# Optimization experiments

Measured on AMD Instinct MI355X. Metric: run time of the kernel, lower is better.

Reference implementation:

```python
import jax, jax.numpy as jnp
import numpy as np

B, N, K = 16, 2048, 16          # clouds, points per cloud, knn k
C_IN, C_OUT = 64, 64

def setup_inputs() -> dict:
    key = jax.random.key(0)
    ks = jax.random.split(key, 8)
    s_in = 1.0 / np.sqrt(C_IN)
    return {
        "x": jax.random.normal(ks[0], (B * N, C_IN), jnp.float32),
        "pos": jax.random.normal(ks[1], (B * N, 3), jnp.float32),
        "batch": jnp.repeat(jnp.arange(B, dtype=jnp.int32), N),
        "W_pos": jax.random.normal(ks[2], (3, C_OUT), jnp.float32) / np.sqrt(3.0),
        "b_pos": jnp.zeros((C_OUT,), jnp.float32),
        "W_attn": jax.random.normal(ks[3], (C_OUT, C_OUT), jnp.float32) / np.sqrt(C_OUT),
        "b_attn": jnp.zeros((C_OUT,), jnp.float32),
        "W_val": jax.random.normal(ks[4], (C_IN, C_OUT), jnp.float32) * s_in,
        "W_src": jax.random.normal(ks[5], (C_IN, C_OUT), jnp.float32) * s_in,
        "W_dst": jax.random.normal(ks[6], (C_IN, C_OUT), jnp.float32) * s_in,
    }

def _gather(a, idx):
    # a: [B, N, D], idx: [B, N, K+1] -> [B, N, K+1, D]
    return jax.vmap(lambda ab, ib: ab[ib])(a, idx)

def reference(x, pos, batch, W_pos, b_pos, W_attn, b_attn, W_val, W_src, W_dst):
    # batch is assumed contiguous with equal-size clouds (B clouds of N points),
    # so batch-restricted knn_graph == per-cloud knn after reshape.
    posr = pos.reshape(B, N, 3)
    xr = x.reshape(B, N, C_IN)
    # knn_graph(loop=False): exclude self, then PointTransformerConv re-adds self loops
    d2 = jnp.sum((posr[:, :, None, :] - posr[:, None, :, :]) ** 2, axis=-1)  # [B,N,N]
    d2 = d2 + jnp.eye(N, dtype=d2.dtype) * 1e10
    _, nbr = jax.lax.top_k(-d2, K)                                # [B,N,K] sources j per target i
    self_idx = jnp.broadcast_to(jnp.arange(N)[None, :, None], (B, N, 1))
    nbr = jnp.concatenate([nbr, self_idx], axis=2)                # self loop -> [B,N,K+1]
    alpha_i = xr @ W_dst                                          # lin_dst(x_i)  [B,N,C_OUT]
    alpha_j = _gather(xr @ W_src, nbr)                            # lin_src(x_j)  [B,N,K+1,C_OUT]
    val_j = _gather(xr @ W_val, nbr)                              # lin(x_j)
    pos_j = _gather(posr, nbr)                                    # [B,N,K+1,3]
    delta = (posr[:, :, None, :] - pos_j) @ W_pos + b_pos         # pos_nn(pos_i - pos_j)
    alpha = alpha_i[:, :, None, :] - alpha_j + delta              # subtraction attention
    alpha = alpha @ W_attn + b_attn                               # attn_nn
    alpha = jax.nn.softmax(alpha, axis=2)                         # segment softmax per target i
    out = jnp.sum(alpha * (val_j + delta), axis=2)                # weighted scatter-sum
    return out.reshape(B * N, C_OUT)
```

## Files before the change

### kernel.cpp

```cpp
#include <hip/hip_runtime.h>
#include <math.h>

#define BBATCH 16
#define NPC    2048
#define KNBR   16
#define NPTS   (BBATCH*NPC)
#define NGEMM  512
#define NKNN   512
#define BUFCAP 512

__global__ __launch_bounds__(1024) void prep_kernel(
    const float* __restrict__ Wpos, const float* __restrict__ bpos,
    const float* __restrict__ Wattn, const float* __restrict__ battn,
    const float* __restrict__ Wsrc, const float* __restrict__ Wdst,
    float* __restrict__ Hd, float* __restrict__ Hs,
    float* __restrict__ WP2, float* __restrict__ bb) {
  __shared__ float sW[4096];
  __shared__ float sD[4096];
  __shared__ float sS[4096];
  int t = threadIdx.x;
  ((float4*)sW)[t] = ((const float4*)Wattn)[t];
  ((float4*)sD)[t] = ((const float4*)Wdst)[t];
  ((float4*)sS)[t] = ((const float4*)Wsrc)[t];
  __syncthreads();
  int c = t & 63, r0 = t >> 6;
#pragma unroll
  for (int q = 0; q < 4; ++q) {
    int r = r0 + 16 * q;
    float ad = 0.f, as = 0.f;
    for (int d = 0; d < 64; ++d) {
      float w = sW[d * 64 + c];
      ad += sD[r * 64 + d] * w;
      as += sS[r * 64 + d] * w;
    }
    Hd[r * 64 + c] = ad;
    Hs[r * 64 + c] = as;
  }
  if (t < 64) {
    for (int rr = 0; rr < 3; ++rr) {
      float a = 0.f;
      for (int d = 0; d < 64; ++d) a += Wpos[rr * 64 + d] * sW[d * 64 + t];
      WP2[rr * 64 + t] = a;
    }
    float a = battn[t];
    for (int d = 0; d < 64; ++d) a += bpos[d] * sW[d * 64 + t];
    bb[t] = a;
  }
}

__global__ __launch_bounds__(1024) void fused_gk_kernel(
    const float* __restrict__ pos, const float* __restrict__ x,
    const float* __restrict__ Hd, const float* __restrict__ Hs,
    const float* __restrict__ Wval,
    int* __restrict__ nbr, float* __restrict__ A2, float* __restrict__ S2,
    float* __restrict__ V) {
  __shared__ __align__(16) char smem[65536];
  int t = threadIdx.x;
  int bid = blockIdx.x;
  int c = t & 63, g = t >> 6;

  if (bid < NGEMM) {
    float* R0 = (float*)smem;
    float* R1 = (float*)(smem + 16384);
    float* R2 = (float*)(smem + 32768);
    float* R3 = (float*)(smem + 49152);
    ((float4*)R0)[t] = ((const float4*)(x + (size_t)bid * 64 * 64))[t];
    ((float4*)R1)[t] = ((const float4*)Hd)[t];
    ((float4*)R2)[t] = ((const float4*)Hs)[t];
    ((float4*)R3)[t] = ((const float4*)Wval)[t];
    __syncthreads();

    float v0 = 0, v1 = 0, v2 = 0, v3 = 0;
    float a0 = 0, a1 = 0, a2 = 0, a3 = 0;
    float s0 = 0, s1 = 0, s2 = 0, s3 = 0;
    const float4* xr0 = (const float4*)(R0 + (g * 4 + 0) * 64);
    const float4* xr1 = (const float4*)(R0 + (g * 4 + 1) * 64);
    const float4* xr2 = (const float4*)(R0 + (g * 4 + 2) * 64);
    const float4* xr3 = (const float4*)(R0 + (g * 4 + 3) * 64);
#pragma unroll 4
    for (int k4 = 0; k4 < 16; ++k4) {
      float4 q0 = xr0[k4], q1 = xr1[k4], q2 = xr2[k4], q3 = xr3[k4];
#pragma unroll
      for (int kk = 0; kk < 4; ++kk) {
        int k = k4 * 4 + kk;
        float wv = R3[k * 64 + c];
        float wa = R1[k * 64 + c];
        float ws = R2[k * 64 + c];
        float e0 = (kk == 0) ? q0.x : (kk == 1) ? q0.y : (kk == 2) ? q0.z : q0.w;
        float e1 = (kk == 0) ? q1.x : (kk == 1) ? q1.y : (kk == 2) ? q1.z : q1.w;
        float e2 = (kk == 0) ? q2.x : (kk == 1) ? q2.y : (kk == 2) ? q2.z : q2.w;
        float e3 = (kk == 0) ? q3.x : (kk == 1) ? q3.y : (kk == 2) ? q3.z : q3.w;
        v0 += e0 * wv; v1 += e1 * wv; v2 += e2 * wv; v3 += e3 * wv;
        a0 += e0 * wa; a1 += e1 * wa; a2 += e2 * wa; a3 += e3 * wa;
        s0 += e0 * ws; s1 += e1 * ws; s2 += e2 * ws; s3 += e3 * ws;
      }
    }
    size_t o0 = ((size_t)bid * 64 + g * 4 + 0) * 64 + c;
    V[o0] = v0; A2[o0] = a0; S2[o0] = s0;
    size_t o1 = o0 + 64;  V[o1] = v1; A2[o1] = a1; S2[o1] = s1;
    size_t o2 = o0 + 128; V[o2] = v2; A2[o2] = a2; S2[o2] = s2;
    size_t o3 = o0 + 192; V[o3] = v3; A2[o3] = a3; S2[o3] = s3;
    return;
  }

  int kb = bid - NGEMM;
  float4* pos4 = (float4*)smem;
  unsigned short* buf = (unsigned short*)(smem + 32768);
  int cloud = kb >> 5;
  const float* pc = pos + (size_t)cloud * NPC * 3;
  for (int p = t; p < NPC; p += 1024)
    pos4[p] = make_float4(pc[3 * p], pc[3 * p + 1], pc[3 * p + 2], 0.f);
  __syncthreads();

  int w = g, lane = c;
  for (int u = 0; u < 4; ++u) {
    int lt = u * 16 + w;
    int gi = kb * 64 + lt;
    int ti = gi & (NPC - 1);
    float4 tp = pos4[ti];
    float tx = tp.x, ty = tp.y, tz = tp.z;

    int bkt[32];
#pragma unroll
    for (int cc = 0; cc < 32; ++cc) {
      int j = cc * 64 + lane;
      float4 q = pos4[j];
      float dx = tx - q.x, dy = ty - q.y, dz = tz - q.z;
      float d2 = dx * dx + dy * dy + dz * dz;
      int b = (int)(__float_as_uint(d2) >> 20) - 896;
      bkt[cc] = max(0, min(255, b));
    }

    int lo = 0, hi = 255;
    for (int it = 0; it < 8; ++it) {
      int mid = (lo + hi) >> 1;
      int cnt = 0;
#pragma unroll
      for (int cc = 0; cc < 32; ++cc)
        cnt += (int)__popcll(__ballot(bkt[cc] <= mid));
      if (cnt >= 17) hi = mid; else lo = mid + 1;
    }
    int Tp1 = min(hi + 1, 255);

    int base = 0;
#pragma unroll
    for (int cc = 0; cc < 32; ++cc) {
      bool f = (bkt[cc] <= Tp1);
      unsigned long long mm = __ballot(f);
      unsigned int pre = __builtin_amdgcn_mbcnt_hi(
          (unsigned)(mm >> 32), __builtin_amdgcn_mbcnt_lo((unsigned)mm, 0u));
      if (f) {
        int p = base + (int)pre;
        if (p < BUFCAP) buf[w * BUFCAP + p] = (unsigned short)(cc * 64 + lane);
      }
      base += (int)__popcll(mm);
    }
    int n = min(base, BUFCAP);
    double txd = (double)tx, tyd = (double)ty, tzd = (double)tz;

    if (n <= 64) {
      unsigned long long gb = 0xFFFFFFFFFFFFFFFFull;
      int gj = 0x40000000 + lane;
      if (lane < n) {
        int j = buf[w * BUFCAP + lane];
        if (j != ti) {
          float4 q = pos4[j];
          double dx = __dsub_rn(txd, (double)q.x);
          double dy = __dsub_rn(tyd, (double)q.y);
          double dz = __dsub_rn(tzd, (double)q.z);
          double d2 = __dadd_rn(__dadd_rn(__dmul_rn(dx, dx), __dmul_rn(dy, dy)),
                                __dmul_rn(dz, dz));
          gb = (unsigned long long)__double_as_longlong(d2);
          gj = j;
        }
      }
      for (int k = 2; k <= 64; k <<= 1) {
        for (int jj = k >> 1; jj > 0; jj >>= 1) {
          unsigned long long ob = __shfl_xor(gb, jj);
          int oj = __shfl_xor(gj, jj);
          bool keepmin = (((lane & k) == 0) == ((lane & jj) == 0));
          bool less = (ob < gb) || (ob == gb && oj < gj);
          if (keepmin == less) { gb = ob; gj = oj; }
        }
      }
      if (lane < KNBR) nbr[(size_t)gi * KNBR + lane] = gj;
    } else {
      unsigned long long kb2[8];
      int id2[8];
#pragma unroll
      for (int r = 0; r < 8; ++r) {
        int e = r * 64 + lane;
        kb2[r] = 0xFFFFFFFFFFFFFFFFull;
        id2[r] = 0x40000000 + e;
        if (e < n) {
          int j = buf[w * BUFCAP + e];
          if (j != ti) {
            float4 q = pos4[j];
            double dx = __dsub_rn(txd, (double)q.x);
            double dy = __dsub_rn(tyd, (double)q.y);
            double dz = __dsub_rn(tzd, (double)q.z);
            double d2 = __dadd_rn(
                __dadd_rn(__dmul_rn(dx, dx), __dmul_rn(dy, dy)),
                __dmul_rn(dz, dz));
            kb2[r] = (unsigned long long)__double_as_longlong(d2);
            id2[r] = j;
          }
        }
      }
      for (int r = 0; r < KNBR; ++r) {
        unsigned long long lb = kb2[0];
        int lj = id2[0];
#pragma unroll
        for (int cc = 1; cc < 8; ++cc)
          if (kb2[cc] < lb || (kb2[cc] == lb && id2[cc] < lj)) {
            lb = kb2[cc]; lj = id2[cc];
          }
        unsigned long long gb2 = lb;
        int gj2 = lj;
#pragma unroll
        for (int d = 32; d >= 1; d >>= 1) {
          unsigned long long ob = __shfl_xor(gb2, d);
          int oj = __shfl_xor(gj2, d);
          if (ob < gb2 || (ob == gb2 && oj < gj2)) { gb2 = ob; gj2 = oj; }
        }
#pragma unroll
        for (int cc = 0; cc < 8; ++cc)
          if (id2[cc] == gj2) kb2[cc] = 0xFFFFFFFFFFFFFFFFull;
        if (lane == 0) nbr[(size_t)gi * KNBR + r] = gj2;
      }
    }
  }
}

__global__ __launch_bounds__(256) void edge_kernel(
    const float* __restrict__ pos, const int* __restrict__ nbr,
    const float* __restrict__ A2, const float* __restrict__ S2,
    const float* __restrict__ V, const float* __restrict__ WP2,
    const float* __restrict__ bbv, const float* __restrict__ Wpos,
    const float* __restrict__ bpos, float* __restrict__ out) {
  int t = threadIdx.x, w = t >> 6, c = t & 63;
  int bid = blockIdx.x;
  int xcd = bid & 7, slot = bid >> 3;
  int cloud = xcd + 8 * (slot >> 9);
  int cb = slot & 511;
  int gi = cloud * NPC + cb * 4 + w;
  int cloudbase = gi & ~(NPC - 1);
  float pix = pos[(size_t)gi * 3], piy = pos[(size_t)gi * 3 + 1],
        piz = pos[(size_t)gi * 3 + 2];
  float a2 = A2[(size_t)gi * 64 + c];
  float wp0 = WP2[c], wp1 = WP2[64 + c], wp2 = WP2[128 + c], bbc = bbv[c];
  float u0 = Wpos[c], u1 = Wpos[64 + c], u2 = Wpos[128 + c], bpc = bpos[c];

  float lg[17], vl[17];
#pragma unroll
  for (int e = 0; e < 17; ++e) {
    int j = (e < 16) ? nbr[(size_t)gi * KNBR + e] : (gi & (NPC - 1));
    int jg = cloudbase + j;
    float dx = pix - pos[(size_t)jg * 3];
    float dy = piy - pos[(size_t)jg * 3 + 1];
    float dz = piz - pos[(size_t)jg * 3 + 2];
    float s2 = S2[(size_t)jg * 64 + c];
    float v = V[(size_t)jg * 64 + c];
    lg[e] = a2 - s2 + dx * wp0 + dy * wp1 + dz * wp2 + bbc;
    vl[e] = v + dx * u0 + dy * u1 + dz * u2 + bpc;
  }
  float mx = lg[0];
#pragma unroll
  for (int e = 1; e < 17; ++e) mx = fmaxf(mx, lg[e]);
  float den = 0.f, acc = 0.f;
#pragma unroll
  for (int e = 0; e < 17; ++e) {
    float wgt = __expf(lg[e] - mx);
    den += wgt;
    acc += wgt * vl[e];
  }
  out[(size_t)gi * 64 + c] = acc / den;
}

extern "C" void kernel_launch(void* const* d_in, const int* in_sizes, int n_in,
                              void* d_out, int out_size, void* d_ws, size_t ws_size,
                              hipStream_t stream) {
  const float* x     = (const float*)d_in[0];
  const float* pos   = (const float*)d_in[1];
  const float* Wpos  = (const float*)d_in[3];
  const float* bpos  = (const float*)d_in[4];
  const float* Wattn = (const float*)d_in[5];
  const float* battn = (const float*)d_in[6];
  const float* Wval  = (const float*)d_in[7];
  const float* Wsrc  = (const float*)d_in[8];
  const float* Wdst  = (const float*)d_in[9];

  float* ws  = (float*)d_ws;
  float* A2  = ws;
  float* S2  = A2 + (size_t)NPTS * 64;
  float* V   = S2 + (size_t)NPTS * 64;
  float* WP2 = V + (size_t)NPTS * 64;
  float* bb  = WP2 + 192;
  int*   nbr = (int*)(bb + 64);
  float* Hd  = (float*)(nbr + (size_t)NPTS * KNBR);
  float* Hs  = Hd + 4096;
  float* out = (float*)d_out;

  prep_kernel<<<1, 1024, 0, stream>>>(Wpos, bpos, Wattn, battn, Wsrc, Wdst,
                                      Hd, Hs, WP2, bb);
  fused_gk_kernel<<<NGEMM + NKNN, 1024, 0, stream>>>(
      pos, x, Hd, Hs, Wval, nbr, A2, S2, V);
  edge_kernel<<<NPTS / 4, 256, 0, stream>>>(pos, nbr, A2, S2, V, WP2, bb,
                                            Wpos, bpos, out);
}
```

Measured before the change: 223.5 us.

## Interleave S2/V into one buffer, SoA positions in LDS, linear edge block order

Stores the source-projection and value rows interleaved as float2 in a single buffer, so each neighbor gather in the edge kernel is one 8-byte load instead of two separate 4-byte loads from different arrays. The kNN stage now keeps positions in LDS as separate x/y/z arrays rather than padded float4s, which cuts LDS use and changes the bank access pattern. The edge kernel drops its XCD-aware cloud remapping in favor of a plain linear block-to-point mapping. The last change can lower L2 locality per XCD, since blocks from one cloud are no longer pinned to the same die.

```diff
diff --git a/kernel.cpp b/kernel.cpp
--- a/kernel.cpp
+++ b/kernel.cpp
@@ -52,8 +52,7 @@
     const float* __restrict__ pos, const float* __restrict__ x,
     const float* __restrict__ Hd, const float* __restrict__ Hs,
     const float* __restrict__ Wval,
-    int* __restrict__ nbr, float* __restrict__ A2, float* __restrict__ S2,
-    float* __restrict__ V) {
+    int* __restrict__ nbr, float* __restrict__ A2, float* __restrict__ IL) {
   __shared__ __align__(16) char smem[65536];
   int t = threadIdx.x;
   int bid = blockIdx.x;
@@ -95,21 +94,30 @@
         s0 += e0 * ws; s1 += e1 * ws; s2 += e2 * ws; s3 += e3 * ws;
       }
     }
-    size_t o0 = ((size_t)bid * 64 + g * 4 + 0) * 64 + c;
-    V[o0] = v0; A2[o0] = a0; S2[o0] = s0;
-    size_t o1 = o0 + 64;  V[o1] = v1; A2[o1] = a1; S2[o1] = s1;
-    size_t o2 = o0 + 128; V[o2] = v2; A2[o2] = a2; S2[o2] = s2;
-    size_t o3 = o0 + 192; V[o3] = v3; A2[o3] = a3; S2[o3] = s3;
+    size_t row = (size_t)bid * 64 + g * 4;
+    A2[(row + 0) * 64 + c] = a0;
+    A2[(row + 1) * 64 + c] = a1;
+    A2[(row + 2) * 64 + c] = a2;
+    A2[(row + 3) * 64 + c] = a3;
+    ((float2*)(IL + (row + 0) * 128))[c] = make_float2(s0, v0);
+    ((float2*)(IL + (row + 1) * 128))[c] = make_float2(s1, v1);
+    ((float2*)(IL + (row + 2) * 128))[c] = make_float2(s2, v2);
+    ((float2*)(IL + (row + 3) * 128))[c] = make_float2(s3, v3);
     return;
   }
 
   int kb = bid - NGEMM;
-  float4* pos4 = (float4*)smem;
-  unsigned short* buf = (unsigned short*)(smem + 32768);
+  float* px = (float*)smem;
+  float* py = (float*)(smem + 8192);
+  float* pz = (float*)(smem + 16384);
+  unsigned short* buf = (unsigned short*)(smem + 24576);
   int cloud = kb >> 5;
   const float* pc = pos + (size_t)cloud * NPC * 3;
-  for (int p = t; p < NPC; p += 1024)
-    pos4[p] = make_float4(pc[3 * p], pc[3 * p + 1], pc[3 * p + 2], 0.f);
+  for (int p = t; p < NPC; p += 1024) {
+    px[p] = pc[3 * p];
+    py[p] = pc[3 * p + 1];
+    pz[p] = pc[3 * p + 2];
+  }
   __syncthreads();
 
   int w = g, lane = c;
@@ -117,15 +125,13 @@
     int lt = u * 16 + w;
     int gi = kb * 64 + lt;
     int ti = gi & (NPC - 1);
-    float4 tp = pos4[ti];
-    float tx = tp.x, ty = tp.y, tz = tp.z;
+    float tx = px[ti], ty = py[ti], tz = pz[ti];
 
     int bkt[32];
 #pragma unroll
     for (int cc = 0; cc < 32; ++cc) {
       int j = cc * 64 + lane;
-      float4 q = pos4[j];
-      float dx = tx - q.x, dy = ty - q.y, dz = tz - q.z;
+      float dx = tx - px[j], dy = ty - py[j], dz = tz - pz[j];
       float d2 = dx * dx + dy * dy + dz * dz;
       int b = (int)(__float_as_uint(d2) >> 20) - 896;
       bkt[cc] = max(0, min(255, b));
@@ -164,10 +170,9 @@
       if (lane < n) {
         int j = buf[w * BUFCAP + lane];
         if (j != ti) {
-          float4 q = pos4[j];
-          double dx = __dsub_rn(txd, (double)q.x);
-          double dy = __dsub_rn(tyd, (double)q.y);
-          double dz = __dsub_rn(tzd, (double)q.z);
+          double dx = __dsub_rn(txd, (double)px[j]);
+          double dy = __dsub_rn(tyd, (double)py[j]);
+          double dz = __dsub_rn(tzd, (double)pz[j]);
           double d2 = __dadd_rn(__dadd_rn(__dmul_rn(dx, dx), __dmul_rn(dy, dy)),
                                 __dmul_rn(dz, dz));
           gb = (unsigned long long)__double_as_longlong(d2);
@@ -195,10 +200,9 @@
         if (e < n) {
           int j = buf[w * BUFCAP + e];
           if (j != ti) {
-            float4 q = pos4[j];
-            double dx = __dsub_rn(txd, (double)q.x);
-            double dy = __dsub_rn(tyd, (double)q.y);
-            double dz = __dsub_rn(tzd, (double)q.z);
+            double dx = __dsub_rn(txd, (double)px[j]);
+            double dy = __dsub_rn(tyd, (double)py[j]);
+            double dz = __dsub_rn(tzd, (double)pz[j]);
             double d2 = __dadd_rn(
                 __dadd_rn(__dmul_rn(dx, dx), __dmul_rn(dy, dy)),
                 __dmul_rn(dz, dz));
@@ -234,16 +238,12 @@
 
 __global__ __launch_bounds__(256) void edge_kernel(
     const float* __restrict__ pos, const int* __restrict__ nbr,
-    const float* __restrict__ A2, const float* __restrict__ S2,
-    const float* __restrict__ V, const float* __restrict__ WP2,
-    const float* __restrict__ bbv, const float* __restrict__ Wpos,
-    const float* __restrict__ bpos, float* __restrict__ out) {
+    const float* __restrict__ A2, const float* __restrict__ IL,
+    const float* __restrict__ WP2, const float* __restrict__ bbv,
+    const float* __restrict__ Wpos, const float* __restrict__ bpos,
+    float* __restrict__ out) {
   int t = threadIdx.x, w = t >> 6, c = t & 63;
-  int bid = blockIdx.x;
-  int xcd = bid & 7, slot = bid >> 3;
-  int cloud = xcd + 8 * (slot >> 9);
-  int cb = slot & 511;
-  int gi = cloud * NPC + cb * 4 + w;
+  int gi = blockIdx.x * 4 + w;
   int cloudbase = gi & ~(NPC - 1);
   float pix = pos[(size_t)gi * 3], piy = pos[(size_t)gi * 3 + 1],
         piz = pos[(size_t)gi * 3 + 2];
@@ -259,10 +259,9 @@
     float dx = pix - pos[(size_t)jg * 3];
     float dy = piy - pos[(size_t)jg * 3 + 1];
     float dz = piz - pos[(size_t)jg * 3 + 2];
-    float s2 = S2[(size_t)jg * 64 + c];
-    float v = V[(size_t)jg * 64 + c];
-    lg[e] = a2 - s2 + dx * wp0 + dy * wp1 + dz * wp2 + bbc;
-    vl[e] = v + dx * u0 + dy * u1 + dz * u2 + bpc;
+    float2 sv = *(const float2*)(IL + (size_t)jg * 128 + 2 * c);
+    lg[e] = a2 - sv.x + dx * wp0 + dy * wp1 + dz * wp2 + bbc;
+    vl[e] = sv.y + dx * u0 + dy * u1 + dz * u2 + bpc;
   }
   float mx = lg[0];
 #pragma unroll
@@ -292,9 +291,8 @@
 
   float* ws  = (float*)d_ws;
   float* A2  = ws;
-  float* S2  = A2 + (size_t)NPTS * 64;
-  float* V   = S2 + (size_t)NPTS * 64;
-  float* WP2 = V + (size_t)NPTS * 64;
+  float* IL  = A2 + (size_t)NPTS * 64;
+  float* WP2 = IL + (size_t)NPTS * 128;
   float* bb  = WP2 + 192;
   int*   nbr = (int*)(bb + 64);
   float* Hd  = (float*)(nbr + (size_t)NPTS * KNBR);
@@ -304,7 +302,7 @@
   prep_kernel<<<1, 1024, 0, stream>>>(Wpos, bpos, Wattn, battn, Wsrc, Wdst,
                                       Hd, Hs, WP2, bb);
   fused_gk_kernel<<<NGEMM + NKNN, 1024, 0, stream>>>(
-      pos, x, Hd, Hs, Wval, nbr, A2, S2, V);
-  edge_kernel<<<NPTS / 4, 256, 0, stream>>>(pos, nbr, A2, S2, V, WP2, bb,
+      pos, x, Hd, Hs, Wval, nbr, A2, IL);
+  edge_kernel<<<NPTS / 4, 256, 0, stream>>>(pos, nbr, A2, IL, WP2, bb,
                                             Wpos, bpos, out);
 }
```

After: 279.7 us. 1.25x slower.

## Split fused GEMM/KNN kernel into separate kernels with XCD-aware block mapping

Applied to the files above, without the earlier changes.

Splits the combined GEMM+KNN launch into two separate kernels, each launched with its own grid. Both kernels remap block IDs so that blocks of the same cloud land on the same XCD. The KNN kernel also stores positions as SoA arrays in shared memory instead of padded float4. This is meant to cut the shared-memory footprint and register pressure of the fused kernel and improve cache locality, but it adds a launch and serializes two phases that previously could run concurrently.

```diff
diff --git a/kernel.cpp b/kernel.cpp
--- a/kernel.cpp
+++ b/kernel.cpp
@@ -48,68 +48,79 @@
   }
 }
 
-__global__ __launch_bounds__(1024) void fused_gk_kernel(
-    const float* __restrict__ pos, const float* __restrict__ x,
-    const float* __restrict__ Hd, const float* __restrict__ Hs,
-    const float* __restrict__ Wval,
-    int* __restrict__ nbr, float* __restrict__ A2, float* __restrict__ S2,
-    float* __restrict__ V) {
-  __shared__ __align__(16) char smem[65536];
+__global__ __launch_bounds__(1024, 8) void gemm_kernel(
+    const float* __restrict__ x, const float* __restrict__ Hd,
+    const float* __restrict__ Hs, const float* __restrict__ Wval,
+    float* __restrict__ A2, float* __restrict__ S2, float* __restrict__ V) {
+  __shared__ __align__(16) float smem[16384];
   int t = threadIdx.x;
-  int bid = blockIdx.x;
+  int bid0 = blockIdx.x;
+  int xcd = bid0 & 7, idx = bid0 >> 3;
+  int cloud = xcd + 8 * (idx >> 5);
+  int bid = cloud * 32 + (idx & 31);
   int c = t & 63, g = t >> 6;
 
-  if (bid < NGEMM) {
-    float* R0 = (float*)smem;
-    float* R1 = (float*)(smem + 16384);
-    float* R2 = (float*)(smem + 32768);
-    float* R3 = (float*)(smem + 49152);
-    ((float4*)R0)[t] = ((const float4*)(x + (size_t)bid * 64 * 64))[t];
-    ((float4*)R1)[t] = ((const float4*)Hd)[t];
-    ((float4*)R2)[t] = ((const float4*)Hs)[t];
-    ((float4*)R3)[t] = ((const float4*)Wval)[t];
-    __syncthreads();
-
-    float v0 = 0, v1 = 0, v2 = 0, v3 = 0;
-    float a0 = 0, a1 = 0, a2 = 0, a3 = 0;
-    float s0 = 0, s1 = 0, s2 = 0, s3 = 0;
-    const float4* xr0 = (const float4*)(R0 + (g * 4 + 0) * 64);
-    const float4* xr1 = (const float4*)(R0 + (g * 4 + 1) * 64);
-    const float4* xr2 = (const float4*)(R0 + (g * 4 + 2) * 64);
-    const float4* xr3 = (const float4*)(R0 + (g * 4 + 3) * 64);
+  float* R0 = smem;
+  float* R1 = smem + 4096;
+  float* R2 = smem + 8192;
+  float* R3 = smem + 12288;
+  ((float4*)R0)[t] = ((const float4*)(x + (size_t)bid * 64 * 64))[t];
+  ((float4*)R1)[t] = ((const float4*)Hd)[t];
+  ((float4*)R2)[t] = ((const float4*)Hs)[t];
+  ((float4*)R3)[t] = ((const float4*)Wval)[t];
+  __syncthreads();
+
+  float v0 = 0, v1 = 0, v2 = 0, v3 = 0;
+  float a0 = 0, a1 = 0, a2 = 0, a3 = 0;
+  float s0 = 0, s1 = 0, s2 = 0, s3 = 0;
+  const float4* xr0 = (const float4*)(R0 + (g * 4 + 0) * 64);
+  const float4* xr1 = (const float4*)(R0 + (g * 4 + 1) * 64);
+  const float4* xr2 = (const float4*)(R0 + (g * 4 + 2) * 64);
+  const float4* xr3 = (const float4*)(R0 + (g * 4 + 3) * 64);
 #pragma unroll 4
-    for (int k4 = 0; k4 < 16; ++k4) {
-      float4 q0 = xr0[k4], q1 = xr1[k4], q2 = xr2[k4], q3 = xr3[k4];
-#pragma unroll
-      for (int kk = 0; kk < 4; ++kk) {
-        int k = k4 * 4 + kk;
-        float wv = R3[k * 64 + c];
-        float wa = R1[k * 64 + c];
-        float ws = R2[k * 64 + c];
-        float e0 = (kk == 0) ? q0.x : (kk == 1) ? q0.y : (kk == 2) ? q0.z : q0.w;
-        float e1 = (kk == 0) ? q1.x : (kk == 1) ? q1.y : (kk == 2) ? q1.z : q1.w;
-        float e2 = (kk == 0) ? q2.x : (kk == 1) ? q2.y : (kk == 2) ? q2.z : q2.w;
-        float e3 = (kk == 0) ? q3.x : (kk == 1) ? q3.y : (kk == 2) ? q3.z : q3.w;
-        v0 += e0 * wv; v1 += e1 * wv; v2 += e2 * wv; v3 += e3 * wv;
-        a0 += e0 * wa; a1 += e1 * wa; a2 += e2 * wa; a3 += e3 * wa;
-        s0 += e0 * ws; s1 += e1 * ws; s2 += e2 * ws; s3 += e3 * ws;
-      }
-    }
-    size_t o0 = ((size_t)bid * 64 + g * 4 + 0) * 64 + c;
-    V[o0] = v0; A2[o0] = a0; S2[o0] = s0;
-    size_t o1 = o0 + 64;  V[o1] = v1; A2[o1] = a1; S2[o1] = s1;
-    size_t o2 = o0 + 128; V[o2] = v2; A2[o2] = a2; S2[o2] = s2;
-    size_t o3 = o0 + 192; V[o3] = v3; A2[o3] = a3; S2[o3] = s3;
-    return;
-  }
-
-  int kb = bid - NGEMM;
-  float4* pos4 = (float4*)smem;
-  unsigned short* buf = (unsigned short*)(smem + 32768);
-  int cloud = kb >> 5;
+  for (int k4 = 0; k4 < 16; ++k4) {
+    float4 q0 = xr0[k4], q1 = xr1[k4], q2 = xr2[k4], q3 = xr3[k4];
+#pragma unroll
+    for (int kk = 0; kk < 4; ++kk) {
+      int k = k4 * 4 + kk;
+      float wv = R3[k * 64 + c];
+      float wa = R1[k * 64 + c];
+      float ws = R2[k * 64 + c];
+      float e0 = (kk == 0) ? q0.x : (kk == 1) ? q0.y : (kk == 2) ? q0.z : q0.w;
+      float e1 = (kk == 0) ? q1.x : (kk == 1) ? q1.y : (kk == 2) ? q1.z : q1.w;
+      float e2 = (kk == 0) ? q2.x : (kk == 1) ? q2.y : (kk == 2) ? q2.z : q2.w;
+      float e3 = (kk == 0) ? q3.x : (kk == 1) ? q3.y : (kk == 2) ? q3.z : q3.w;
+      v0 += e0 * wv; v1 += e1 * wv; v2 += e2 * wv; v3 += e3 * wv;
+      a0 += e0 * wa; a1 += e1 * wa; a2 += e2 * wa; a3 += e3 * wa;
+      s0 += e0 * ws; s1 += e1 * ws; s2 += e2 * ws; s3 += e3 * ws;
+    }
+  }
+  size_t o0 = ((size_t)bid * 64 + g * 4 + 0) * 64 + c;
+  V[o0] = v0; A2[o0] = a0; S2[o0] = s0;
+  size_t o1 = o0 + 64;  V[o1] = v1; A2[o1] = a1; S2[o1] = s1;
+  size_t o2 = o0 + 128; V[o2] = v2; A2[o2] = a2; S2[o2] = s2;
+  size_t o3 = o0 + 192; V[o3] = v3; A2[o3] = a3; S2[o3] = s3;
+}
+
+__global__ __launch_bounds__(1024, 8) void knn_kernel(
+    const float* __restrict__ pos, int* __restrict__ nbr) {
+  __shared__ float px[NPC];
+  __shared__ float py[NPC];
+  __shared__ float pz[NPC];
+  __shared__ unsigned short buf[16 * BUFCAP];
+  int t = threadIdx.x;
+  int bid0 = blockIdx.x;
+  int xcd = bid0 & 7, idx = bid0 >> 3;
+  int cloud = xcd + 8 * (idx >> 5);
+  int kb = cloud * 32 + (idx & 31);
+  int c = t & 63, g = t >> 6;
+
   const float* pc = pos + (size_t)cloud * NPC * 3;
-  for (int p = t; p < NPC; p += 1024)
-    pos4[p] = make_float4(pc[3 * p], pc[3 * p + 1], pc[3 * p + 2], 0.f);
+  for (int p = t; p < NPC; p += 1024) {
+    px[p] = pc[3 * p];
+    py[p] = pc[3 * p + 1];
+    pz[p] = pc[3 * p + 2];
+  }
   __syncthreads();
 
   int w = g, lane = c;
@@ -117,15 +128,13 @@
     int lt = u * 16 + w;
     int gi = kb * 64 + lt;
     int ti = gi & (NPC - 1);
-    float4 tp = pos4[ti];
-    float tx = tp.x, ty = tp.y, tz = tp.z;
+    float tx = px[ti], ty = py[ti], tz = pz[ti];
 
     int bkt[32];
 #pragma unroll
     for (int cc = 0; cc < 32; ++cc) {
       int j = cc * 64 + lane;
-      float4 q = pos4[j];
-      float dx = tx - q.x, dy = ty - q.y, dz = tz - q.z;
+      float dx = tx - px[j], dy = ty - py[j], dz = tz - pz[j];
       float d2 = dx * dx + dy * dy + dz * dz;
       int b = (int)(__float_as_uint(d2) >> 20) - 896;
       bkt[cc] = max(0, min(255, b));
@@ -164,10 +173,9 @@
       if (lane < n) {
         int j = buf[w * BUFCAP + lane];
         if (j != ti) {
-          float4 q = pos4[j];
-          double dx = __dsub_rn(txd, (double)q.x);
-          double dy = __dsub_rn(tyd, (double)q.y);
-          double dz = __dsub_rn(tzd, (double)q.z);
+          double dx = __dsub_rn(txd, (double)px[j]);
+          double dy = __dsub_rn(tyd, (double)py[j]);
+          double dz = __dsub_rn(tzd, (double)pz[j]);
           double d2 = __dadd_rn(__dadd_rn(__dmul_rn(dx, dx), __dmul_rn(dy, dy)),
                                 __dmul_rn(dz, dz));
           gb = (unsigned long long)__double_as_longlong(d2);
@@ -195,10 +203,9 @@
         if (e < n) {
           int j = buf[w * BUFCAP + e];
           if (j != ti) {
-            float4 q = pos4[j];
-            double dx = __dsub_rn(txd, (double)q.x);
-            double dy = __dsub_rn(tyd, (double)q.y);
-            double dz = __dsub_rn(tzd, (double)q.z);
+            double dx = __dsub_rn(txd, (double)px[j]);
+            double dy = __dsub_rn(tyd, (double)py[j]);
+            double dz = __dsub_rn(tzd, (double)pz[j]);
             double d2 = __dadd_rn(
                 __dadd_rn(__dmul_rn(dx, dx), __dmul_rn(dy, dy)),
                 __dmul_rn(dz, dz));
@@ -242,9 +249,8 @@
   int bid = blockIdx.x;
   int xcd = bid & 7, slot = bid >> 3;
   int cloud = xcd + 8 * (slot >> 9);
-  int cb = slot & 511;
-  int gi = cloud * NPC + cb * 4 + w;
-  int cloudbase = gi & ~(NPC - 1);
+  int gi = cloud * NPC + (slot & 511) * 4 + w;
+  int cloudbase = cloud * NPC;
   float pix = pos[(size_t)gi * 3], piy = pos[(size_t)gi * 3 + 1],
         piz = pos[(size_t)gi * 3 + 2];
   float a2 = A2[(size_t)gi * 64 + c];
@@ -303,8 +309,8 @@
 
   prep_kernel<<<1, 1024, 0, stream>>>(Wpos, bpos, Wattn, battn, Wsrc, Wdst,
                                       Hd, Hs, WP2, bb);
-  fused_gk_kernel<<<NGEMM + NKNN, 1024, 0, stream>>>(
-      pos, x, Hd, Hs, Wval, nbr, A2, S2, V);
+  knn_kernel<<<NKNN, 1024, 0, stream>>>(pos, nbr);
+  gemm_kernel<<<NGEMM, 1024, 0, stream>>>(x, Hd, Hs, Wval, A2, S2, V);
   edge_kernel<<<NPTS / 4, 256, 0, stream>>>(pos, nbr, A2, S2, V, WP2, bb,
                                             Wpos, bpos, out);
 }
```

New measurement: 315.7 us. +41.3%, slower.

## Stage cloud positions in LDS and use online softmax in edge kernel

Applied to the files above, without the earlier changes.

The edge kernel now runs 512-thread blocks that each handle 32 target points of one cloud. Each block first copies that cloud's full position array (24 KB) into shared memory, then reads neighbour positions from LDS instead of global memory. Neighbour indices are loaded once per wavefront and broadcast with shuffles, and the two-pass softmax becomes a streaming online softmax with no 17-element register arrays. The cost is a per-block preload of all 2048 positions, which is redundant across the 64 blocks per cloud, and the XCD-aware block-to-cloud mapping is dropped, which may hurt L2 locality.

```diff
diff --git a/kernel.cpp b/kernel.cpp
--- a/kernel.cpp
+++ b/kernel.cpp
@@ -232,49 +232,55 @@
   }
 }
 
-__global__ __launch_bounds__(256) void edge_kernel(
+__global__ __launch_bounds__(512) void edge_kernel(
     const float* __restrict__ pos, const int* __restrict__ nbr,
     const float* __restrict__ A2, const float* __restrict__ S2,
     const float* __restrict__ V, const float* __restrict__ WP2,
     const float* __restrict__ bbv, const float* __restrict__ Wpos,
     const float* __restrict__ bpos, float* __restrict__ out) {
-  int t = threadIdx.x, w = t >> 6, c = t & 63;
+  __shared__ float lp[NPC * 3];
+  int t = threadIdx.x;
   int bid = blockIdx.x;
-  int xcd = bid & 7, slot = bid >> 3;
-  int cloud = xcd + 8 * (slot >> 9);
-  int cb = slot & 511;
-  int gi = cloud * NPC + cb * 4 + w;
-  int cloudbase = gi & ~(NPC - 1);
-  float pix = pos[(size_t)gi * 3], piy = pos[(size_t)gi * 3 + 1],
-        piz = pos[(size_t)gi * 3 + 2];
-  float a2 = A2[(size_t)gi * 64 + c];
+  int cloud = bid >> 6;
+  int tb = (bid & 63) * 32;
+  const float4* pc4 = (const float4*)(pos + (size_t)cloud * NPC * 3);
+#pragma unroll
+  for (int r = 0; r < 3; ++r) ((float4*)lp)[t + 512 * r] = pc4[t + 512 * r];
+  __syncthreads();
+
+  int w = t >> 6, c = t & 63;
   float wp0 = WP2[c], wp1 = WP2[64 + c], wp2 = WP2[128 + c], bbc = bbv[c];
   float u0 = Wpos[c], u1 = Wpos[64 + c], u2 = Wpos[128 + c], bpc = bpos[c];
-
-  float lg[17], vl[17];
-#pragma unroll
-  for (int e = 0; e < 17; ++e) {
-    int j = (e < 16) ? nbr[(size_t)gi * KNBR + e] : (gi & (NPC - 1));
-    int jg = cloudbase + j;
-    float dx = pix - pos[(size_t)jg * 3];
-    float dy = piy - pos[(size_t)jg * 3 + 1];
-    float dz = piz - pos[(size_t)jg * 3 + 2];
-    float s2 = S2[(size_t)jg * 64 + c];
-    float v = V[(size_t)jg * 64 + c];
-    lg[e] = a2 - s2 + dx * wp0 + dy * wp1 + dz * wp2 + bbc;
-    vl[e] = v + dx * u0 + dy * u1 + dz * u2 + bpc;
-  }
-  float mx = lg[0];
-#pragma unroll
-  for (int e = 1; e < 17; ++e) mx = fmaxf(mx, lg[e]);
-  float den = 0.f, acc = 0.f;
-#pragma unroll
-  for (int e = 0; e < 17; ++e) {
-    float wgt = __expf(lg[e] - mx);
-    den += wgt;
-    acc += wgt * vl[e];
-  }
-  out[(size_t)gi * 64 + c] = acc / den;
+  size_t cbase = (size_t)cloud * NPC;
+
+  for (int u = 0; u < 4; ++u) {
+    int ti = tb + u * 8 + w;
+    size_t gi = cbase + ti;
+    int jv = nbr[gi * KNBR + (c & 15)];
+    float pix = lp[3 * ti], piy = lp[3 * ti + 1], piz = lp[3 * ti + 2];
+    float a2 = A2[gi * 64 + c];
+
+    float m = -1e30f, den = 0.f, acc = 0.f;
+#pragma unroll
+    for (int e = 0; e < 17; ++e) {
+      int j = (e < 16) ? __shfl(jv, e) : ti;
+      float dx = pix - lp[3 * j];
+      float dy = piy - lp[3 * j + 1];
+      float dz = piz - lp[3 * j + 2];
+      size_t jg = cbase + j;
+      float s2 = S2[jg * 64 + c];
+      float v = V[jg * 64 + c];
+      float lg = a2 - s2 + dx * wp0 + dy * wp1 + dz * wp2 + bbc;
+      float vl = v + dx * u0 + dy * u1 + dz * u2 + bpc;
+      float mn = fmaxf(m, lg);
+      float sc = __expf(m - mn);
+      float wgt = __expf(lg - mn);
+      den = den * sc + wgt;
+      acc = acc * sc + wgt * vl;
+      m = mn;
+    }
+    out[gi * 64 + c] = acc / den;
+  }
 }
 
 extern "C" void kernel_launch(void* const* d_in, const int* in_sizes, int n_in,
@@ -305,6 +311,6 @@
                                       Hd, Hs, WP2, bb);
   fused_gk_kernel<<<NGEMM + NKNN, 1024, 0, stream>>>(
       pos, x, Hd, Hs, Wval, nbr, A2, S2, V);
-  edge_kernel<<<NPTS / 4, 256, 0, stream>>>(pos, nbr, A2, S2, V, WP2, bb,
-                                            Wpos, bpos, out);
+  edge_kernel<<<NPTS / 32, 512, 0, stream>>>(pos, nbr, A2, S2, V, WP2, bb,
+                                             Wpos, bpos, out);
 }
```

Result: no change. 226.4 us (+1.3%).
